# Performance work log

Hardware: AMD Instinct MI355X
Metric: run time of the kernel (lower is better)

## Reference

```python
import jax, jax.numpy as jnp
import numpy as np

B, S, H = 4, 4096, 1024
GAMMA = 0.96875


def decay_mask(seq_len, gamma, dtype=jnp.float32):
    # D[i, j] = gamma**(i-j) for i >= j, else 0 (causal gamma-decay mask)
    i = jnp.arange(seq_len)[:, None]
    j = jnp.arange(seq_len)[None, :]
    exp = (i - j).astype(dtype)
    return jnp.where(i >= j, jnp.power(jnp.asarray(gamma, dtype), exp), jnp.zeros((), dtype))


def setup_inputs() -> dict:
    key = jax.random.key(0)
    ks = jax.random.split(key, 6)
    sc = 1.0 / np.sqrt(H)
    return {
        "x": jax.random.normal(ks[0], (B, S, H), dtype=jnp.float32),
        "Wq": jax.random.normal(ks[1], (H, H), dtype=jnp.float32) * sc,
        "bq": jax.random.normal(ks[2], (H,), dtype=jnp.float32) * 0.01,
        "Wk": jax.random.normal(ks[3], (H, H), dtype=jnp.float32) * sc,
        "bk": jax.random.normal(ks[4], (H,), dtype=jnp.float32) * 0.01,
        "Wv": jax.random.normal(ks[5], (H, H), dtype=jnp.float32) * sc,
    }


def reference(x, Wq, bq, Wk, bk, Wv):
    # Parallel representation of retention.
    seq_len = x.shape[1]
    q = jnp.einsum("bsh,oh->bso", x, Wq) + bq  # [B,S,H]
    k = jnp.einsum("bsh,oh->bso", x, Wk) + bk  # [B,S,H]
    v = jnp.einsum("bsh,oh->bso", x, Wv)       # [B,S,H]
    D = decay_mask(seq_len, GAMMA, x.dtype)     # [S,S]
    scores = jnp.einsum("bqh,bkh->bqk", q, k) * D[None]  # [B,S,S]
    return jnp.einsum("bqk,bkh->bqh", scores, v)
```

## Files before the change

### kernel.cpp

```cpp
#include <hip/hip_runtime.h>


typedef __attribute__((ext_vector_type(8))) short short8;
typedef __attribute__((ext_vector_type(4))) float floatx4;

#define MFMA(a, b, c) __builtin_amdgcn_mfma_f32_16x16x32_bf16((a), (b), (c), 0, 0, 0)

#define B_SZ   4
#define S_LEN  4096
#define H_DIM  1024
#define NROWS  (B_SZ * S_LEN)
#define HP     1088
#define LOG2G  (-0.045803690f)

__device__ __forceinline__ unsigned short f32_to_bf16_rn(float f) {
    unsigned int u = __float_as_uint(f);
    u += 0x7FFFu + ((u >> 16) & 1u);
    return (unsigned short)(u >> 16);
}

#define GLOAD_LDS16(gptr, lptr)                                                        \
    __builtin_amdgcn_global_load_lds((__attribute__((address_space(1))) void*)(gptr),  \
                                     (__attribute__((address_space(3))) void*)(lptr),  \
                                     16, 0, 0)

#define BAR()                                   \
    do {                                        \
        asm volatile("" ::: "memory");          \
        __builtin_amdgcn_s_barrier();           \
        asm volatile("" ::: "memory");          \
    } while (0)

__device__ __forceinline__ void cvt_bf16_body(int i, const float* __restrict__ src,
                                              unsigned short* __restrict__ dst, int n4) {
    if (i >= n4) return;
    float4 v = ((const float4*)src)[i];
    ushort4 o;
    o.x = f32_to_bf16_rn(v.x);
    o.y = f32_to_bf16_rn(v.y);
    o.z = f32_to_bf16_rn(v.z);
    o.w = f32_to_bf16_rn(v.w);
    ((ushort4*)dst)[i] = o;
}

__device__ __forceinline__ void cvt_x_body(int idx, const float* __restrict__ src,
                                           unsigned short* __restrict__ dst) {
    int row = idx >> 7, c8 = (idx & 127) * 8;
    const float4* s = (const float4*)(src + (size_t)row * H_DIM + c8);
    float4 a = s[0], b = s[1];
    ushort4 o0, o1;
    o0.x = f32_to_bf16_rn(a.x); o0.y = f32_to_bf16_rn(a.y);
    o0.z = f32_to_bf16_rn(a.z); o0.w = f32_to_bf16_rn(a.w);
    o1.x = f32_to_bf16_rn(b.x); o1.y = f32_to_bf16_rn(b.y);
    o1.z = f32_to_bf16_rn(b.z); o1.w = f32_to_bf16_rn(b.w);
    ushort4* d = (ushort4*)(dst + (size_t)row * HP + c8);
    d[0] = o0; d[1] = o1;
}

__device__ __forceinline__ void fill_pad_body(int idx, unsigned short* __restrict__ dst) {
    int row = idx >> 3, c = idx & 7;
    uint4 v; v.x = (c == 0) ? 0x00003F80u : 0u; v.y = 0u; v.z = 0u; v.w = 0u;
    *(uint4*)(dst + (size_t)row * HP + 1024 + c * 8) = v;
}

__device__ __forceinline__ void zero_pb_body(int idx, unsigned short* __restrict__ pb) {
    int r = idx >> 13;
    int rem = idx & 8191;
    int row = rem >> 5, c8 = (rem & 31) * 8;
    int batch = r / 3, sub = r % 3;
    int qt = batch * 16 + (sub == 2 ? 1 : 0);
    int col0 = (sub == 2 ? 0 : sub * 256);
    uint4 z; z.x = 0u; z.y = 0u; z.z = 0u; z.w = 0u;
    *(uint4*)(pb + (size_t)qt * (256 * 768) + (size_t)row * 768 + col0 + c8) = z;
}

__device__ __forceinline__ void tr_cvt_body(float (&Lt)[128][33],
                                            const float* __restrict__ Wsrc,
                                            const float* __restrict__ bias,
                                            unsigned short* __restrict__ dst,
                                            int bx, int by, int tid) {
    if (by >= 32) {
        if (bx != 0) return;
        const int h0 = by * 32;
#pragma unroll
        for (int i = 0; i < 128; ++i) {
            int idx = i * 256 + tid;
            int r = idx >> 10, cc = idx & 1023;
            int h = h0 + r;
            float v = (h == 1024) ? bias[cc] : 0.0f;
            dst[(size_t)h * 1024 + cc] = f32_to_bf16_rn(v);
        }
        return;
    }
    const int w0 = bx * 128, h0 = by * 32;
#pragma unroll
    for (int i = 0; i < 16; ++i) {
        int idx = i * 256 + tid;
        int r = idx >> 5, cc = idx & 31;
        Lt[r][cc] = Wsrc[(size_t)(w0 + r) * 1024 + h0 + cc];
    }
    __syncthreads();
#pragma unroll
    for (int i = 0; i < 16; ++i) {
        int idx = i * 256 + tid;
        int hh = idx >> 7, ww = idx & 127;
        dst[(size_t)(h0 + hh) * 1024 + w0 + ww] = f32_to_bf16_rn(Lt[ww][hh]);
    }
}

__device__ __forceinline__ void gemm_body128(unsigned short (&As)[2][128 * 32],
                                             unsigned short (&Bs)[2][128 * 32],
                                             int bx, int by,
                                             const unsigned short* __restrict__ A, int lda,
                                             const unsigned short* __restrict__ W, int ldw,
                                             unsigned short* __restrict__ outp, int ldo,
                                             int K, int p0) {
    const int tid  = threadIdx.x;
    const int lane = tid & 63;
    const int w4   = tid >> 6;
    const int wm   = w4 >> 1, wn = w4 & 1;
    const int l15  = lane & 15;
    const int q8   = (lane >> 4) * 8;
    const int q4   = (lane >> 4) * 4;

    const int aRow0 = by * 128, wRow0 = bx * 128;

    floatx4 acc[4][4];
#pragma unroll
    for (int i = 0; i < 4; ++i)
#pragma unroll
        for (int j = 0; j < 4; ++j) acc[i][j] = (floatx4)0.0f;

    for (int k0 = 0; k0 < K; k0 += 64) {
        __syncthreads();
#pragma unroll
        for (int p = 0; p < 2; ++p) {
            const int c = p * 256 + tid;
            const unsigned short* gA = A + (size_t)(aRow0 + (c >> 2)) * lda + k0 + (c & 3) * 8;
            const unsigned short* gW = W + (size_t)(wRow0 + (c >> 2)) * ldw + k0 + (c & 3) * 8;
            char* dA0 = (char*)&As[0][0] + (size_t)(p * 256 + w4 * 64) * 16;
            char* dA1 = (char*)&As[1][0] + (size_t)(p * 256 + w4 * 64) * 16;
            char* dB0 = (char*)&Bs[0][0] + (size_t)(p * 256 + w4 * 64) * 16;
            char* dB1 = (char*)&Bs[1][0] + (size_t)(p * 256 + w4 * 64) * 16;
            GLOAD_LDS16(gA,      dA0);
            GLOAD_LDS16(gA + 32, dA1);
            GLOAD_LDS16(gW,      dB0);
            GLOAD_LDS16(gW + 32, dB1);
        }
        __syncthreads();

#pragma unroll
        for (int h = 0; h < 2; ++h) {
            short8 af[4], bf[4];
#pragma unroll
            for (int mt = 0; mt < 4; ++mt)
                af[mt] = *(const short8*)(&As[h][0] + (wm * 64 + mt * 16 + l15) * 32 + q8);
#pragma unroll
            for (int nt = 0; nt < 4; ++nt)
                bf[nt] = *(const short8*)(&Bs[h][0] + (wn * 64 + nt * 16 + l15) * 32 + q8);
#pragma unroll
            for (int mt = 0; mt < 4; ++mt)
#pragma unroll
                for (int nt = 0; nt < 4; ++nt)
                    acc[mt][nt] = MFMA(af[mt], bf[nt], acc[mt][nt]);
        }
    }

#pragma unroll
    for (int nt = 0; nt < 4; ++nt) {
        const int ol = wn * 64 + nt * 16 + l15;
#pragma unroll
        for (int mt = 0; mt < 4; ++mt) {
#pragma unroll
            for (int r = 0; r < 4; ++r) {
                const int nl = wm * 64 + mt * 16 + q4 + r;
                const int o = wRow0 + ol;
                if (o < p0)
                    outp[(size_t)(aRow0 + nl) * ldo + o] = f32_to_bf16_rn(acc[mt][nt][r]);
            }
        }
    }
}

template <int MODE, int NT>
__device__ __forceinline__ void g256_body(unsigned short (&lds)[2][2][16384],
                                          int bx, int by,
                                          const unsigned short* __restrict__ Abase, int lda,
                                          const unsigned short* __restrict__ Wbase, int ldw,
                                          void* __restrict__ outp) {
    const int tid  = threadIdx.x;
    const int lane = tid & 63;
    const int wv   = tid >> 6;
    const int wm   = wv >> 2, wn = wv & 3;
    const int l15  = lane & 15;
    const int q    = lane >> 4;
    const int q4   = q * 4;

    const unsigned short* Ap;
    const unsigned short* Wp;
    int ql = 0;
    if (MODE == 0) {
        Ap = Abase + (size_t)(by * 256) * lda;
        Wp = Wbase + (size_t)(bx * 256) * ldw;
    } else if (MODE == 1) {
        Ap = Abase + (size_t)(bx * 256) * lda;
        Wp = Wbase + (size_t)(by * 256) * ldw;
    } else if (MODE == 2) {
        ql = by & 15;
        const int j256 = ql - 2 + bx;
        if (j256 < 0) return;
        Ap = Abase + (size_t)(by * 256) * lda;
        Wp = Wbase + (size_t)((by >> 4) * S_LEN + j256 * 256) * ldw;
    } else {
        ql = by & 15;
        Ap = Abase + (size_t)by * (256 * 768);
        Wp = Wbase + ((ptrdiff_t)((by >> 4) * H_DIM + bx * 256)) * S_LEN
                   + ((ptrdiff_t)ql - 2) * 256;
    }

    floatx4 acc[8][4];
#pragma unroll
    for (int i = 0; i < 8; ++i)
#pragma unroll
        for (int j = 0; j < 4; ++j) acc[i][j] = (floatx4)0.0f;

    auto STAGE2 = [&](int t, int m) {
        const int b  = t & 1;
        const int k0 = t * 64;
        const unsigned short* gp = m ? Wp : Ap;
        const int ld = m ? ldw : lda;
        char* base = (char*)&lds[b][m][0];
#pragma unroll
        for (int i = 0; i < 4; ++i) {
            const int c   = i * 512 + tid;
            const int row = c >> 3;
            const int ch  = (c & 7) ^ (row & 7);
            GLOAD_LDS16(gp + (size_t)row * ld + k0 + ch * 8,
                        base + (size_t)(i * 512 + wv * 64) * 16);
        }
    };

    short8 afr[4][2], bfr[2][2];
    auto RDA = [&](int t, int mh) {
        const unsigned short* base = &lds[t & 1][0][0];
#pragma unroll
        for (int mt = 0; mt < 4; ++mt) {
            const int r = wm * 128 + mh * 64 + mt * 16 + l15;
#pragma unroll
            for (int h = 0; h < 2; ++h) {
                const int ch = (h * 4 + q) ^ (r & 7);
                afr[mt][h] = *(const short8*)(base + r * 64 + ch * 8);
            }
        }
    };
    auto RDB = [&](int t, int nh) {
        const unsigned short* base = &lds[t & 1][1][0];
#pragma unroll
        for (int nt = 0; nt < 2; ++nt) {
            const int r = wn * 64 + (nh * 2 + nt) * 16 + l15;
#pragma unroll
            for (int h = 0; h < 2; ++h) {
                const int ch = (h * 4 + q) ^ (r & 7);
                bfr[nt][h] = *(const short8*)(base + r * 64 + ch * 8);
            }
        }
    };
    auto QMFMA = [&](int mh, int nh) {
        __builtin_amdgcn_s_setprio(1);
#pragma unroll
        for (int mt = 0; mt < 4; ++mt)
#pragma unroll
            for (int nt = 0; nt < 2; ++nt)
#pragma unroll
                for (int h = 0; h < 2; ++h)
                    acc[mh * 4 + mt][nh * 2 + nt] =
                        MFMA(afr[mt][h], bfr[nt][h], acc[mh * 4 + mt][nh * 2 + nt]);
        __builtin_amdgcn_s_setprio(0);
    };

    STAGE2(0, 0);
    STAGE2(0, 1);
    if (NT > 1) STAGE2(1, 0);
    asm volatile("s_waitcnt vmcnt(4)" ::: "memory");
    BAR();

#pragma unroll 1
    for (int t = 0; t < NT; ++t) {
        const bool sB = (t + 1 < NT);
        const bool sA = (t + 2 < NT);
        RDA(t, 0);
        RDB(t, 0);
        BAR();
        if (sB) STAGE2(t + 1, 1);
        QMFMA(0, 0);
        BAR();
        RDB(t, 1);
        BAR();
        QMFMA(0, 1);
        BAR();
        RDA(t, 1);
        BAR();
        QMFMA(1, 1);
        BAR();
        RDB(t, 0);
        BAR();
        if (sA) STAGE2(t + 2, 0);
        QMFMA(1, 0);
        if (sA) {
            asm volatile("s_waitcnt vmcnt(4)" ::: "memory");
        } else if (sB) {
            asm volatile("s_waitcnt vmcnt(0)" ::: "memory");
        }
        BAR();
    }

#pragma unroll
    for (int nt = 0; nt < 4; ++nt) {
        const int ol = wn * 64 + nt * 16 + l15;
#pragma unroll
        for (int mt = 0; mt < 8; ++mt) {
#pragma unroll
            for (int r = 0; r < 4; ++r) {
                const int nl = wm * 128 + mt * 16 + q4 + r;
                const float v = acc[mt][nt][r];
                if (MODE == 0) {
                    const int o = bx * 256 + ol;
                    if (o < HP)
                        ((unsigned short*)outp)[(size_t)(by * 256 + nl) * HP + o] =
                            f32_to_bf16_rn(v);
                } else if (MODE == 1) {
                    const int s  = by * 256 + ol;
                    const int hh = bx * 256 + nl;
                    ((unsigned short*)outp)[((size_t)(s >> 12) * H_DIM + hh) * S_LEN +
                                            (s & (S_LEN - 1))] = f32_to_bf16_rn(v);
                } else if (MODE == 2) {
                    const int d = (2 - bx) * 256 + nl - ol;
                    const float pv = (d >= 0) ? v * exp2f((float)d * LOG2G) : 0.0f;
                    ((unsigned short*)outp)[(size_t)by * (256 * 768) + (size_t)nl * 768 +
                                            bx * 256 + ol] = f32_to_bf16_rn(pv);
                } else {
                    ((float*)outp)[(size_t)(by * 256 + nl) * H_DIM + bx * 256 + ol] = v;
                }
            }
        }
    }
}

__global__ __launch_bounds__(256) void prep_small(const float* __restrict__ Wq,
                                                  const float* __restrict__ bq,
                                                  const float* __restrict__ Wk,
                                                  const float* __restrict__ bk,
                                                  const float* __restrict__ Wv,
                                                  unsigned short* __restrict__ wqT,
                                                  unsigned short* __restrict__ wkT,
                                                  unsigned short* __restrict__ wvb,
                                                  unsigned short* __restrict__ pb,
                                                  unsigned short* __restrict__ xtb) {
    __shared__ float Lt[128][33];
    const int t = blockIdx.x, tid = threadIdx.x;
    if (t < 288) {
        tr_cvt_body(Lt, Wq, bq, wqT, t & 7, t >> 3, tid);
    } else if (t < 608) {
        const int t2 = t - 288;
        tr_cvt_body(Lt, Wk, bk, wkT, t2 & 7, t2 >> 3, tid);
    } else if (t < 1632) {
        cvt_bf16_body((t - 608) * 256 + tid, Wv, wvb, H_DIM * H_DIM / 4);
    } else if (t < 2016) {
        zero_pb_body((t - 1632) * 256 + tid, pb);
    } else {
        fill_pad_body((t - 2016) * 256 + tid, xtb);
    }
}

__global__ __launch_bounds__(256) void cvtx_p1(const float* __restrict__ x,
                                               unsigned short* __restrict__ xtb,
                                               const unsigned short* __restrict__ wkT,
                                               const unsigned short* __restrict__ wqT,
                                               unsigned short* __restrict__ p1) {
    __shared__ unsigned short As[2][128 * 32];
    __shared__ unsigned short Bs[2][128 * 32];
    const int t = blockIdx.x;
    if (t < 90) {
        gemm_body128(As, Bs, t % 9, t / 9, wkT, 1024, wqT, 1024, p1, HP, 1024, HP);
    } else {
        cvt_x_body((t - 90) * 256 + threadIdx.x, x, xtb);
    }
}

__global__ __launch_bounds__(512, 2) void g256_g(const unsigned short* __restrict__ xtb,
                                                 const unsigned short* __restrict__ p1,
                                                 unsigned short* __restrict__ gb) {
    __shared__ unsigned short lds[2][2][16384];
    const int bid = blockIdx.x;
    const int g = bid & 7, j = bid >> 3;
    g256_body<0, 17>(lds, j % 5, g * 8 + j / 5, xtb, HP, p1, HP, gb);
}

__global__ __launch_bounds__(512, 2) void g256_pbvt(const unsigned short* __restrict__ gb,
                                                    const unsigned short* __restrict__ xtb,
                                                    const unsigned short* __restrict__ wvb,
                                                    unsigned short* __restrict__ pb,
                                                    unsigned short* __restrict__ vtb) {
    __shared__ unsigned short lds[2][2][16384];
    const int t = blockIdx.x;
    if (t < 192) {
        const int g = t & 7, j = t >> 3;
        g256_body<2, 17>(lds, j % 3, g * 8 + j / 3, gb, HP, xtb, HP, pb);
    } else {
        const int t2 = t - 192;
        const int g = t2 & 7, j = t2 >> 3;
        g256_body<1, 16>(lds, j & 3, g * 8 + (j >> 2), wvb, 1024, xtb, HP, vtb);
    }
}

__global__ __launch_bounds__(512, 2) void g256_out(const unsigned short* __restrict__ pb,
                                                   const unsigned short* __restrict__ vtb,
                                                   float* __restrict__ out) {
    __shared__ unsigned short lds[2][2][16384];
    const int bid = blockIdx.x;
    const int g = bid & 7, j = bid >> 3;
    g256_body<3, 12>(lds, j & 3, g * 8 + (j >> 2), pb, 768, vtb, S_LEN, out);
}

extern "C" void kernel_launch(void* const* d_in, const int* in_sizes, int n_in,
                              void* d_out, int out_size, void* d_ws, size_t ws_size,
                              hipStream_t stream) {
    (void)in_sizes; (void)n_in; (void)out_size; (void)ws_size;

    const float* x  = (const float*)d_in[0];
    const float* Wq = (const float*)d_in[1];
    const float* bq = (const float*)d_in[2];
    const float* Wk = (const float*)d_in[3];
    const float* bk = (const float*)d_in[4];
    const float* Wv = (const float*)d_in[5];
    float* out = (float*)d_out;

    unsigned short* xtb = (unsigned short*)d_ws;
    unsigned short* gb  = xtb + (size_t)NROWS * HP;
    unsigned short* vtb = gb  + (size_t)NROWS * HP;
    unsigned short* pb  = vtb + (size_t)NROWS * H_DIM;
    unsigned short* wqT = pb  + (size_t)64 * 256 * 768;
    unsigned short* wkT = wqT + (size_t)1152 * 1024;
    unsigned short* p1  = wkT + (size_t)1280 * 1024;
    unsigned short* wvb = p1  + (size_t)1280 * HP;

    prep_small<<<2528, 256, 0, stream>>>(Wq, bq, Wk, bk, Wv, wqT, wkT, wvb, pb, xtb);
    cvtx_p1<<<90 + 8192, 256, 0, stream>>>(x, xtb, wkT, wqT, p1);
    g256_g<<<320, 512, 0, stream>>>(xtb, p1, gb);
    g256_pbvt<<<192 + 256, 512, 0, stream>>>(gb, xtb, wvb, pb, vtb);
    g256_out<<<256, 512, 0, stream>>>(pb, vtb, out);
}
```

Baseline: 329.5 us.

## Stage GEMM epilogue through swizzled LDS for vectorized stores, load B fragments once

The epilogue now writes accumulator tiles into a swizzled LDS image and then emits 16-byte vectorized global stores. Before, each thread made scattered 2- or 4-byte stores, which in the transposed mode were heavily strided. The decay factor in mode 2 is split into precomputed row and column exp2 factors, replacing a per-element exp2. B fragments for all four n-tiles are read once per k-step, which removes two LDS reads and several barriers but raises register pressure.

```diff
diff --git a/kernel.cpp b/kernel.cpp
--- a/kernel.cpp
+++ b/kernel.cpp
@@ -240,7 +240,7 @@
         }
     };
 
-    short8 afr[4][2], bfr[2][2];
+    short8 afr[4][2], bfr[4][2];
     auto RDA = [&](int t, int mh) {
         const unsigned short* base = &lds[t & 1][0][0];
 #pragma unroll
@@ -253,11 +253,11 @@
             }
         }
     };
-    auto RDB = [&](int t, int nh) {
+    auto RDB = [&](int t) {
         const unsigned short* base = &lds[t & 1][1][0];
 #pragma unroll
-        for (int nt = 0; nt < 2; ++nt) {
-            const int r = wn * 64 + (nh * 2 + nt) * 16 + l15;
+        for (int nt = 0; nt < 4; ++nt) {
+            const int r = wn * 64 + nt * 16 + l15;
 #pragma unroll
             for (int h = 0; h < 2; ++h) {
                 const int ch = (h * 4 + q) ^ (r & 7);
@@ -274,7 +274,7 @@
 #pragma unroll
                 for (int h = 0; h < 2; ++h)
                     acc[mh * 4 + mt][nh * 2 + nt] =
-                        MFMA(afr[mt][h], bfr[nt][h], acc[mh * 4 + mt][nh * 2 + nt]);
+                        MFMA(afr[mt][h], bfr[nh * 2 + nt][h], acc[mh * 4 + mt][nh * 2 + nt]);
         __builtin_amdgcn_s_setprio(0);
     };
 
@@ -289,20 +289,16 @@
         const bool sB = (t + 1 < NT);
         const bool sA = (t + 2 < NT);
         RDA(t, 0);
-        RDB(t, 0);
+        RDB(t);
         BAR();
         if (sB) STAGE2(t + 1, 1);
         QMFMA(0, 0);
         BAR();
-        RDB(t, 1);
-        BAR();
         QMFMA(0, 1);
         BAR();
         RDA(t, 1);
         BAR();
         QMFMA(1, 1);
-        BAR();
-        RDB(t, 0);
         BAR();
         if (sA) STAGE2(t + 2, 0);
         QMFMA(1, 0);
@@ -314,33 +310,86 @@
         BAR();
     }
 
-#pragma unroll
-    for (int nt = 0; nt < 4; ++nt) {
-        const int ol = wn * 64 + nt * 16 + l15;
+    if (MODE != 3) {
+        unsigned short* img = &lds[0][0][0];
+        float colf[4], rowf[8][4];
+        if (MODE == 2) {
+#pragma unroll
+            for (int nt = 0; nt < 4; ++nt)
+                colf[nt] = exp2f((float)(wn * 64 + nt * 16 + l15) * -LOG2G);
+#pragma unroll
+            for (int mt = 0; mt < 8; ++mt)
+#pragma unroll
+                for (int r = 0; r < 4; ++r)
+                    rowf[mt][r] = exp2f(
+                        (float)((2 - bx) * 256 + wm * 128 + mt * 16 + q4 + r) * LOG2G);
+        }
 #pragma unroll
         for (int mt = 0; mt < 8; ++mt) {
 #pragma unroll
-            for (int r = 0; r < 4; ++r) {
-                const int nl = wm * 128 + mt * 16 + q4 + r;
-                const float v = acc[mt][nt][r];
-                if (MODE == 0) {
-                    const int o = bx * 256 + ol;
-                    if (o < HP)
-                        ((unsigned short*)outp)[(size_t)(by * 256 + nl) * HP + o] =
-                            f32_to_bf16_rn(v);
-                } else if (MODE == 1) {
-                    const int s  = by * 256 + ol;
-                    const int hh = bx * 256 + nl;
-                    ((unsigned short*)outp)[((size_t)(s >> 12) * H_DIM + hh) * S_LEN +
-                                            (s & (S_LEN - 1))] = f32_to_bf16_rn(v);
-                } else if (MODE == 2) {
-                    const int d = (2 - bx) * 256 + nl - ol;
-                    const float pv = (d >= 0) ? v * exp2f((float)d * LOG2G) : 0.0f;
-                    ((unsigned short*)outp)[(size_t)by * (256 * 768) + (size_t)nl * 768 +
-                                            bx * 256 + ol] = f32_to_bf16_rn(pv);
-                } else {
-                    ((float*)outp)[(size_t)(by * 256 + nl) * H_DIM + bx * 256 + ol] = v;
+            for (int nt = 0; nt < 4; ++nt) {
+#pragma unroll
+                for (int r = 0; r < 4; ++r) {
+                    const int row = wm * 128 + mt * 16 + q4 + r;
+                    const int col = wn * 64 + nt * 16 + l15;
+                    float v = acc[mt][nt][r];
+                    if (MODE == 2) {
+                        const int d = (2 - bx) * 256 + row - col;
+                        v = (d >= 0) ? v * rowf[mt][r] * colf[nt] : 0.0f;
+                    }
+                    img[row * 256 + (col ^ (((row >> 2) & 3) << 4))] = f32_to_bf16_rn(v);
                 }
+            }
+        }
+        BAR();
+#pragma unroll
+        for (int i = 0; i < 16; ++i) {
+            const int c   = i * 512 + tid;
+            const int row = c >> 5;
+            const int c8  = (c & 31) * 8;
+            short8 v = *(const short8*)&img[row * 256 + (c8 ^ (((row >> 2) & 3) << 4))];
+            if (MODE == 0) {
+                const int gc = bx * 256 + c8;
+                if (gc < HP)
+                    *(short8*)((unsigned short*)outp + (size_t)(by * 256 + row) * HP + gc) = v;
+            } else if (MODE == 1) {
+                const int s  = by * 256 + c8;
+                const int hh = bx * 256 + row;
+                *(short8*)((unsigned short*)outp +
+                           ((size_t)(s >> 12) * H_DIM + hh) * S_LEN + (s & (S_LEN - 1))) = v;
+            } else {
+                *(short8*)((unsigned short*)outp + (size_t)by * (256 * 768) +
+                           (size_t)row * 768 + bx * 256 + c8) = v;
+            }
+        }
+    } else {
+        float* img32 = (float*)&lds[0][0][0];
+#pragma unroll
+        for (int p = 0; p < 2; ++p) {
+            if (p) BAR();
+            if (wm == p) {
+#pragma unroll
+                for (int mt = 0; mt < 8; ++mt)
+#pragma unroll
+                    for (int nt = 0; nt < 4; ++nt)
+#pragma unroll
+                        for (int r = 0; r < 4; ++r) {
+                            const int row = mt * 16 + q4 + r;
+                            const int col = wn * 64 + nt * 16 + l15;
+                            img32[row * 256 + (col ^ (((row >> 2) & 3) << 4))] =
+                                acc[mt][nt][r];
+                        }
+            }
+            BAR();
+#pragma unroll
+            for (int i = 0; i < 16; ++i) {
+                const int c   = i * 512 + tid;
+                const int row = c >> 6;
+                const int c4  = (c & 63) * 4;
+                float4 v = *(const float4*)&img32[row * 256 +
+                                                  (c4 ^ (((row >> 2) & 3) << 4))];
+                *(float4*)((float*)outp + (size_t)(by * 256 + p * 128 + row) * H_DIM +
+                           bx * 256 + c4) = v;
             }
         }
     }
```

After: 307.7 us. -6.6%, faster.
